# Optimization experiments

Hardware: AMD Instinct MI355X
Metric: run time of the kernel (lower is better)

The kernel has to match this reference:

```python
import jax, jax.numpy as jnp
import numpy as np

H = 128          # hidden_size == in_channels == graph_hidden_size
P = 16           # pair_neurons
B = 4096         # number of graph pairs
T = 262144       # total nodes per side
V_D, V_P, V_A = 10000, 4000, 4000          # leaf vocab sizes
NG_D, NG_P, NG_A = 13000, 5200, 5200       # DAG graph node counts
L_D, L_P, L_A = 4, 4, 5                    # ancestor levels
TOTAL_V = V_D + V_P + V_A                  # 18000 rows in all_embedding


def setup_inputs() -> dict:
    key = jax.random.key(0)
    ks = jax.random.split(key, 40)
    n = lambda i, shape, s: jax.random.normal(ks[i], shape, jnp.float32) * s
    ri = lambda i, shape, hi: jax.random.randint(ks[i], shape, 0, hi, dtype=jnp.int64)
    inp = {}
    # forward args
    inp["left_x"] = ri(0, (T, 1), TOTAL_V)
    inp["left_graph_index"] = ri(1, (B,), B)
    inp["right_x"] = ri(2, (T, 1), TOTAL_V)
    inp["right_graph_index"] = ri(3, (B,), B)
    inp["left_x_batch"] = jnp.sort(ri(4, (T,), B))
    inp["right_x_batch"] = jnp.sort(ri(5, (T,), B))
    inp["left_diag_cnt"] = ri(6, (B,), 64)
    inp["right_diag_cnt"] = ri(7, (B,), 64)
    # DAG structure buffers (built by build_ancestors in the original)
    inp["anc_d"] = ri(8, (V_D, L_D), NG_D)
    inp["leaf_d"] = ri(9, (V_D, L_D), NG_D)
    inp["anc_p"] = ri(10, (V_P, L_P), NG_P)
    inp["leaf_p"] = ri(11, (V_P, L_P), NG_P)
    inp["anc_a"] = ri(12, (V_A, L_A), NG_A)
    inp["leaf_a"] = ri(13, (V_A, L_A), NG_A)
    # learned parameters
    inp["emb_d"] = n(14, (NG_D, H), 0.1)
    inp["emb_p"] = n(15, (NG_P, H), 0.1)
    inp["emb_a"] = n(16, (NG_A, H), 0.1)
    inp["Wl_d"] = n(17, (H, 2 * H), 0.05); inp["bl_d"] = n(18, (H,), 0.05); inp["ap_d"] = n(19, (H, 1), 0.05)
    inp["Wl_p"] = n(20, (H, 2 * H), 0.05); inp["bl_p"] = n(21, (H,), 0.05); inp["ap_p"] = n(22, (H, 1), 0.05)
    inp["Wl_a"] = n(23, (H, 2 * H), 0.05); inp["bl_a"] = n(24, (H,), 0.05); inp["ap_a"] = n(25, (H, 1), 0.05)
    inp["W_ntn"] = n(26, (H, H, P), 0.02)
    inp["V_ntn"] = n(27, (P, 2 * H), 0.02)
    inp["b_ntn"] = n(28, (P,), 0.02)
    inp["w_fc"] = n(29, (1, P), 0.1)
    inp["b_fc"] = n(30, (1,), 0.1)
    return inp


def _dag_embedding(emb, anc, leaf, Wl, bl, ap):
    # emb: [Ng,H]; anc/leaf: [V,L] int
    anc_e = emb[anc]    # [V,L,H]
    leaf_e = emb[leaf]  # [V,L,H]
    h = jnp.tanh(jnp.concatenate([anc_e, leaf_e], axis=-1) @ Wl.T + bl)  # [V,L,H]
    aw = (h @ ap)[..., 0]                     # [V,L]
    s = jax.nn.softmax(aw, axis=-1)           # [V,L]
    # torch.matmul((V,L),(V,L,C)).sum(dim=1) == einsum('l,vlc->vc', s.sum(0), anc_e)
    return jnp.einsum('l,vlc->vc', s.sum(axis=0), anc_e)  # [V,H]


def reference(left_x, left_graph_index, right_x, right_graph_index,
              left_x_batch, right_x_batch, left_diag_cnt, right_diag_cnt,
              anc_d, leaf_d, anc_p, leaf_p, anc_a, leaf_a,
              emb_d, emb_p, emb_a,
              Wl_d, bl_d, ap_d, Wl_p, bl_p, ap_p, Wl_a, bl_a, ap_a,
              W_ntn, V_ntn, b_ntn, w_fc, b_fc):
    all_emb = jnp.concatenate([
        _dag_embedding(emb_d, anc_d, leaf_d, Wl_d, bl_d, ap_d),
        _dag_embedding(emb_p, anc_p, leaf_p, Wl_p, bl_p, ap_p),
        _dag_embedding(emb_a, anc_a, leaf_a, Wl_a, bl_a, ap_a),
    ], axis=0)                                  # [TOTAL_V, H]
    left_onto = all_emb[left_x[:, 0]]           # [T,H]
    right_onto = all_emb[right_x[:, 0]]         # [T,H]
    le = jax.ops.segment_sum(left_onto, left_x_batch, num_segments=B)    # [B,H]
    re = jax.ops.segment_sum(right_onto, right_x_batch, num_segments=B)  # [B,H]
    # Neural tensor similarity: tanh(e1^T W_k e2 + V [e1;e2] + b)
    bilinear = jnp.einsum('bi,ijp,bj->bp', le, W_ntn, re)                # [B,P]
    block = jnp.concatenate([le, re], axis=-1) @ V_ntn.T                 # [B,P]
    pair_sim = jnp.tanh(bilinear + block + b_ntn)                        # [B,P]
    out = jax.nn.sigmoid(pair_sim @ w_fc.T + b_fc)[:, 0]                 # [B]
    return out
```

## Files before the change

kernel.cpp:

```cpp
#include <hip/hip_runtime.h>
#include <hip/hip_bf16.h>

typedef __hip_bfloat16 bf16;
typedef __attribute__((ext_vector_type(8))) short bf16x8;
typedef __attribute__((ext_vector_type(4))) float f32x4;

#define HID 128
#define PD  16
#define BB  4096
#define TT  262144
#define VD  10000
#define VP  4000
#define VA  4000
#define NGD 13000
#define NGP 5200
#define NGA 5200

#define NB_D ((NGD + 31) / 32)
#define NB_P ((NGP + 31) / 32)
#define NB_A ((NGA + 31) / 32)

__device__ __forceinline__ float2 bf2x(unsigned int u) {
    float lo = __uint_as_float(u << 16);
    float hi = __uint_as_float(u & 0xffff0000u);
    return make_float2(lo, hi);
}

union Pack2 { bf16 h[2]; unsigned int u; };
__device__ __forceinline__ unsigned int pk2(float a, float b) {
    Pack2 p; p.h[0] = __float2bfloat16(a); p.h[1] = __float2bfloat16(b); return p.u;
}
__device__ __forceinline__ short bfs(float x) {
    bf16 h = __float2bfloat16(x);
    return *reinterpret_cast<short*>(&h);
}
union FragU { short s[8]; bf16x8 v; uint4 u; };

__global__ __launch_bounds__(256) void prologue(
    const float* __restrict__ Wl_d, const float* __restrict__ Wl_p, const float* __restrict__ Wl_a,
    bf16* __restrict__ B3_d, bf16* __restrict__ B3_p, bf16* __restrict__ B3_a,
    const int* __restrict__ lb, const int* __restrict__ rb,
    int* __restrict__ segL, int* __restrict__ segR, float* __restrict__ s_sum,
    const float* __restrict__ W2,
    bf16* __restrict__ W3h, bf16* __restrict__ W3m, bf16* __restrict__ W3l)
{
    __shared__ float LW[128][17];
    const int bx = blockIdx.x;
    const int tid = threadIdx.x;
    if (bx < 48) {
        const int sec = bx >> 4, jt = bx & 15;
        const float* Wl = (sec == 0) ? Wl_d : (sec == 1) ? Wl_p : Wl_a;
        bf16* B3 = (sec == 0) ? B3_d : (sec == 1) ? B3_p : B3_a;
        const int q = tid >> 6, lane = tid & 63;
        const int quad = lane >> 4, m = lane & 15;
        const int col = jt * 16 + m;
        const float* src = (col < 128) ? (Wl + col * 256) : (Wl + (col - 128) * 256 + 128);
        unsigned int pk[4];
#pragma unroll
        for (int jp = 0; jp < 4; ++jp) {
            int k0 = q * 32 + quad * 8 + 2 * jp;
            pk[jp] = pk2(src[k0], src[k0 + 1]);
        }
        uint4 val = make_uint4(pk[0], pk[1], pk[2], pk[3]);
        *reinterpret_cast<uint4*>(B3 + ((size_t)(jt * 4 + q) * 64 + lane) * 8) = val;
    } else if (bx < 81) {
        int gid = (bx - 48) * 256 + tid;
        if (gid >= 2 * BB + 8 && gid < 2 * BB + 24) s_sum[gid - (2 * BB + 8)] = 0.f;
        const int* batch;
        int* segp;
        int b;
        if (gid <= BB) { batch = lb; segp = segL; b = gid; }
        else if (gid <= 2 * BB + 1) { batch = rb; segp = segR; b = gid - BB - 1; }
        else return;
        int l = 0, r = TT;
        while (l < r) { int m2 = (l + r) >> 1; if (batch[m2] < b) l = m2 + 1; else r = m2; }
        segp[b] = l;
    } else {
        const int t = bx - 81;
        for (int idx = tid; idx < 2048; idx += 256) {
            int k = idx >> 4, m = idx & 15;
            LW[k][m] = W2[(size_t)k * 2048 + 16 * t + m];
        }
        __syncthreads();
        const int q = tid >> 6, lane = tid & 63;
        const int m = lane & 15, quad = lane >> 4;
        FragU fh, fm, fl;
#pragma unroll
        for (int j = 0; j < 8; ++j) {
            float x = LW[32 * q + quad * 8 + j][m];
            bf16 h = __float2bfloat16(x);
            float r = x - __bfloat162float(h);
            bf16 md = __float2bfloat16(r);
            float r2 = r - __bfloat162float(md);
            fh.s[j] = *reinterpret_cast<short*>(&h);
            fm.s[j] = *reinterpret_cast<short*>(&md);
            fl.s[j] = bfs(r2);
        }
        size_t off = ((size_t)(t * 4 + q) * 64 + lane) * 8;
        *reinterpret_cast<uint4*>(W3h + off) = fh.u;
        *reinterpret_cast<uint4*>(W3m + off) = fm.u;
        *reinterpret_cast<uint4*>(W3l + off) = fl.u;
    }
}

__device__ __forceinline__ void stage1_body(
    unsigned short (*Abf)[136],
    const float* __restrict__ emb, const bf16* __restrict__ B3,
    bf16* __restrict__ U, int NG, int blk)
{
    const int tid  = threadIdx.x;
    const int row0 = blk * 32;
    {
        const int r = tid >> 3, seg = tid & 7;
        const int g = row0 + r;
        float v[16];
        if (g < NG) {
            const float4* src = reinterpret_cast<const float4*>(emb + (size_t)g * HID + seg * 16);
#pragma unroll
            for (int i = 0; i < 4; ++i) {
                float4 f = src[i];
                v[4 * i] = f.x; v[4 * i + 1] = f.y; v[4 * i + 2] = f.z; v[4 * i + 3] = f.w;
            }
        } else {
#pragma unroll
            for (int i = 0; i < 16; ++i) v[i] = 0.f;
        }
        unsigned int pk[8];
#pragma unroll
        for (int i = 0; i < 8; ++i) pk[i] = pk2(v[2 * i], v[2 * i + 1]);
        uint4* dst = reinterpret_cast<uint4*>(&Abf[r][seg * 16]);
        dst[0] = make_uint4(pk[0], pk[1], pk[2], pk[3]);
        dst[1] = make_uint4(pk[4], pk[5], pk[6], pk[7]);
    }
    __syncthreads();

    const int lane   = tid & 63;
    const int w      = tid >> 6;
    const int gtile  = w & 1;
    const int jstrip = w >> 1;
    const int lrow   = gtile * 16 + (lane & 15);
    const int koff   = (lane >> 4) * 8;
    const bf16x8* B3f = reinterpret_cast<const bf16x8*>(B3);

    f32x4 acc[8];
#pragma unroll
    for (int t = 0; t < 8; ++t) acc[t] = (f32x4){0.f, 0.f, 0.f, 0.f};

#pragma unroll
    for (int q = 0; q < 4; ++q) {
        bf16x8 ef = *reinterpret_cast<const bf16x8*>(&Abf[lrow][q * 32 + koff]);
#pragma unroll
        for (int t = 0; t < 8; ++t) {
            int jt = jstrip * 8 + t;
            bf16x8 wf = B3f[(jt * 4 + q) * 64 + lane];
            acc[t] = __builtin_amdgcn_mfma_f32_16x16x32_bf16(wf, ef, acc[t], 0, 0, 0);
        }
    }

    const int g = row0 + gtile * 16 + (lane & 15);
    if (g < NG) {
        const int quad = lane >> 4;
        bf16* Ur = U + (size_t)g * 256;
#pragma unroll
        for (int t = 0; t < 8; ++t) {
            int j0 = (jstrip * 8 + t) * 16 + quad * 4;
            uint2 st = make_uint2(pk2(acc[t].x, acc[t].y), pk2(acc[t].z, acc[t].w));
            *reinterpret_cast<uint2*>(Ur + j0) = st;
        }
    }
}

__global__ __launch_bounds__(256) void stage1_mfma(
    const float* __restrict__ emb_d, const bf16* __restrict__ B3_d, bf16* __restrict__ U_d,
    const float* __restrict__ emb_p, const bf16* __restrict__ B3_p, bf16* __restrict__ U_p,
    const float* __restrict__ emb_a, const bf16* __restrict__ B3_a, bf16* __restrict__ U_a)
{
    __shared__ unsigned short Abf[32][136];
    int bx = blockIdx.x;
    if (bx < NB_D)             stage1_body(Abf, emb_d, B3_d, U_d, NGD, bx);
    else if (bx < NB_D + NB_P) stage1_body(Abf, emb_p, B3_p, U_p, NGP, bx - NB_D);
    else                       stage1_body(Abf, emb_a, B3_a, U_a, NGA, bx - NB_D - NB_P);
}

template <int L>
__device__ __forceinline__ void aw_body(
    float* sacc,
    const bf16* __restrict__ U, const int* __restrict__ anc, const int* __restrict__ leaf,
    const float* __restrict__ bl, const float* __restrict__ ap,
    float* __restrict__ s_out, int V, int blk, int nblk)
{
    const int tid  = threadIdx.x;
    const int lane = tid & 63;
    const int wid  = blk * 4 + (tid >> 6);
    const int nw   = nblk * 4;
    const float2 blv = *reinterpret_cast<const float2*>(bl + 2 * lane);
    const float2 apv = *reinterpret_cast<const float2*>(ap + 2 * lane);
    const unsigned int* Uw = reinterpret_cast<const unsigned int*>(U);
    float wacc[L];
#pragma unroll
    for (int l = 0; l < L; ++l) wacc[l] = 0.f;

    for (int vp = wid; vp < V / 2; vp += nw) {
        const int v0 = 2 * vp;
        int a0[L], f0[L], a1[L], f1[L];
        if (L == 4) {
            int4 ia = *reinterpret_cast<const int4*>(anc  + (size_t)v0 * 4);
            int4 ib = *reinterpret_cast<const int4*>(anc  + (size_t)v0 * 4 + 4);
            int4 fa = *reinterpret_cast<const int4*>(leaf + (size_t)v0 * 4);
            int4 fb = *reinterpret_cast<const int4*>(leaf + (size_t)v0 * 4 + 4);
            a0[0] = ia.x; a0[1] = ia.y; a0[2] = ia.z; a0[3] = ia.w;
            a1[0] = ib.x; a1[1] = ib.y; a1[2] = ib.z; a1[3] = ib.w;
            f0[0] = fa.x; f0[1] = fa.y; f0[2] = fa.z; f0[3] = fa.w;
            f1[0] = fb.x; f1[1] = fb.y; f1[2] = fb.z; f1[3] = fb.w;
        } else {
#pragma unroll
            for (int l = 0; l < L; ++l) {
                a0[l] = anc[(size_t)v0 * L + l];
                a1[l] = anc[(size_t)(v0 + 1) * L + l];
                f0[l] = leaf[(size_t)v0 * L + l];
                f1[l] = leaf[(size_t)(v0 + 1) * L + l];
            }
        }
        unsigned int ua0[L], ul0[L], ua1[L], ul1[L];
#pragma unroll
        for (int l = 0; l < L; ++l) {
            ua0[l] = Uw[(size_t)a0[l] * 128 + lane];
            ul0[l] = Uw[(size_t)f0[l] * 128 + 64 + lane];
            ua1[l] = Uw[(size_t)a1[l] * 128 + lane];
            ul1[l] = Uw[(size_t)f1[l] * 128 + 64 + lane];
        }
        float aw0[L], aw1[L];
#pragma unroll
        for (int l = 0; l < L; ++l) {
            float2 x0 = bf2x(ua0[l]), y0 = bf2x(ul0[l]);
            float2 x1 = bf2x(ua1[l]), y1 = bf2x(ul1[l]);
            float p0 = tanhf(x0.x + y0.x + blv.x) * apv.x + tanhf(x0.y + y0.y + blv.y) * apv.y;
            float p1 = tanhf(x1.x + y1.x + blv.x) * apv.x + tanhf(x1.y + y1.y + blv.y) * apv.y;
#pragma unroll
            for (int off = 32; off; off >>= 1) {
                p0 += __shfl_xor(p0, off, 64);
                p1 += __shfl_xor(p1, off, 64);
            }
            aw0[l] = p0; aw1[l] = p1;
        }
        float m0 = aw0[0], m1 = aw1[0];
#pragma unroll
        for (int l = 1; l < L; ++l) { m0 = fmaxf(m0, aw0[l]); m1 = fmaxf(m1, aw1[l]); }
        float d0 = 0.f, d1 = 0.f, e0[L], e1[L];
#pragma unroll
        for (int l = 0; l < L; ++l) {
            e0[l] = __expf(aw0[l] - m0); d0 += e0[l];
            e1[l] = __expf(aw1[l] - m1); d1 += e1[l];
        }
        float i0 = 1.f / d0, i1 = 1.f / d1;
#pragma unroll
        for (int l = 0; l < L; ++l) wacc[l] += e0[l] * i0 + e1[l] * i1;
    }
    if (lane == 0) {
#pragma unroll
        for (int l = 0; l < L; ++l) atomicAdd(&sacc[l], wacc[l]);
    }
    __syncthreads();
    if (tid < L) atomicAdd(&s_out[tid], sacc[tid]);
}

__global__ __launch_bounds__(256) void aw_all(
    const bf16* __restrict__ U_d, const int* __restrict__ anc_d, const int* __restrict__ leaf_d,
    const float* __restrict__ bl_d, const float* __restrict__ ap_d,
    const bf16* __restrict__ U_p, const int* __restrict__ anc_p, const int* __restrict__ leaf_p,
    const float* __restrict__ bl_p, const float* __restrict__ ap_p,
    const bf16* __restrict__ U_a, const int* __restrict__ anc_a, const int* __restrict__ leaf_a,
    const float* __restrict__ bl_a, const float* __restrict__ ap_a,
    float* __restrict__ s_sum)
{
    __shared__ float sacc[5];
    const int tid = threadIdx.x;
    if (tid < 5) sacc[tid] = 0.f;
    __syncthreads();
    int bx = blockIdx.x;
    if (bx < 512)      aw_body<4>(sacc, U_d, anc_d, leaf_d, bl_d, ap_d, s_sum + 0, VD, bx, 512);
    else if (bx < 768) aw_body<4>(sacc, U_p, anc_p, leaf_p, bl_p, ap_p, s_sum + 4, VP, bx - 512, 256);
    else               aw_body<5>(sacc, U_a, anc_a, leaf_a, bl_a, ap_a, s_sum + 8, VA, bx - 768, 256);
}

template <int L>
__device__ __forceinline__ void allemb_body(
    const float* __restrict__ emb, const int* __restrict__ anc,
    const float* __restrict__ s, float* __restrict__ out, int V, int blk, int nblk)
{
    const int tid   = threadIdx.x;
    const int lane4 = tid & 31;
    const int vslot = tid >> 5;
    const float4* emb4 = reinterpret_cast<const float4*>(emb);
    float4* out4 = reinterpret_cast<float4*>(out);
    float sv[L];
#pragma unroll
    for (int l = 0; l < L; ++l) sv[l] = s[l];
    for (int vp = blk * 8 + vslot; vp < V / 2; vp += nblk * 8) {
        const int v0 = 2 * vp;
        int a0[L], a1[L];
        if (L == 4) {
            int4 ia = *reinterpret_cast<const int4*>(anc + (size_t)v0 * 4);
            int4 ib = *reinterpret_cast<const int4*>(anc + (size_t)v0 * 4 + 4);
            a0[0] = ia.x; a0[1] = ia.y; a0[2] = ia.z; a0[3] = ia.w;
            a1[0] = ib.x; a1[1] = ib.y; a1[2] = ib.z; a1[3] = ib.w;
        } else {
#pragma unroll
            for (int l = 0; l < L; ++l) {
                a0[l] = anc[(size_t)v0 * L + l];
                a1[l] = anc[(size_t)(v0 + 1) * L + l];
            }
        }
        float4 e0[L], e1[L];
#pragma unroll
        for (int l = 0; l < L; ++l) {
            e0[l] = emb4[(size_t)a0[l] * 32 + lane4];
            e1[l] = emb4[(size_t)a1[l] * 32 + lane4];
        }
        float4 r0 = make_float4(0.f, 0.f, 0.f, 0.f);
        float4 r1 = make_float4(0.f, 0.f, 0.f, 0.f);
#pragma unroll
        for (int l = 0; l < L; ++l) {
            r0.x += sv[l] * e0[l].x; r0.y += sv[l] * e0[l].y;
            r0.z += sv[l] * e0[l].z; r0.w += sv[l] * e0[l].w;
            r1.x += sv[l] * e1[l].x; r1.y += sv[l] * e1[l].y;
            r1.z += sv[l] * e1[l].z; r1.w += sv[l] * e1[l].w;
        }
        out4[(size_t)v0 * 32 + lane4]       = r0;
        out4[(size_t)(v0 + 1) * 32 + lane4] = r1;
    }
}

__global__ __launch_bounds__(256) void allemb_all(
    const float* __restrict__ emb_d, const int* __restrict__ anc_d,
    const float* __restrict__ emb_p, const int* __restrict__ anc_p,
    const float* __restrict__ emb_a, const int* __restrict__ anc_a,
    const float* __restrict__ s_sum, float* __restrict__ all_emb)
{
    int bx = blockIdx.x;
    if (bx < 512)
        allemb_body<4>(emb_d, anc_d, s_sum + 0, all_emb, VD, bx, 512);
    else if (bx < 768)
        allemb_body<4>(emb_p, anc_p, s_sum + 4, all_emb + (size_t)VD * HID, VP, bx - 512, 256);
    else
        allemb_body<5>(emb_a, anc_a, s_sum + 8, all_emb + (size_t)(VD + VP) * HID, VA, bx - 768, 256);
}

__global__ __launch_bounds__(256) void segsum_mlp(
    const float* __restrict__ all_emb,
    const int* __restrict__ lx, const int* __restrict__ segL, float* __restrict__ le,
    const int* __restrict__ rx, const int* __restrict__ segR, float* __restrict__ re)
{
    __shared__ float4 red[4][32];
    const int tid  = threadIdx.x;
    const int b    = blockIdx.x & (BB - 1);
    const int lane = tid & 63;
    const int w    = tid >> 6;
    const int* x;
    const int* seg;
    float* out;
    if (blockIdx.x < BB) { x = lx; seg = segL; out = le; }
    else                 { x = rx; seg = segR; out = re; }
    const int lo = seg[b], hi = seg[b + 1];
    const int half  = lane >> 5;
    const int lane4 = lane & 31;
    const float4* AE4 = reinterpret_cast<const float4*>(all_emb);
    float4 acc = make_float4(0.f, 0.f, 0.f, 0.f);

    for (int tb = lo + 16 * w; tb < hi; tb += 64) {
        int idxv = x[min(tb + (lane & 15), hi - 1)];
        float4 v[8];
        int val[8];
#pragma unroll
        for (int u = 0; u < 8; ++u) {
            int src = 2 * u + half;
            int ridx = __shfl(idxv, src, 64);
            val[u] = (tb + src) < hi;
            v[u] = AE4[(size_t)ridx * 32 + lane4];
        }
#pragma unroll
        for (int u = 0; u < 8; ++u) {
            if (val[u]) {
                acc.x += v[u].x; acc.y += v[u].y;
                acc.z += v[u].z; acc.w += v[u].w;
            }
        }
    }
    acc.x += __shfl_xor(acc.x, 32, 64);
    acc.y += __shfl_xor(acc.y, 32, 64);
    acc.z += __shfl_xor(acc.z, 32, 64);
    acc.w += __shfl_xor(acc.w, 32, 64);
    if (lane < 32) red[w][lane4] = acc;
    __syncthreads();
    if (tid < 32) {
        float4 r0 = red[0][tid], r1 = red[1][tid], r2 = red[2][tid], r3 = red[3][tid];
        float4 s;
        s.x = r0.x + r1.x + r2.x + r3.x;
        s.y = r0.y + r1.y + r2.y + r3.y;
        s.z = r0.z + r1.z + r2.z + r3.z;
        s.w = r0.w + r1.w + r2.w + r3.w;
        reinterpret_cast<float4*>(out)[(size_t)b * 32 + tid] = s;
    }
}

__global__ __launch_bounds__(256) void ntn_mfma(
    const float* __restrict__ le, const float* __restrict__ re,
    const bf16* __restrict__ W3h, const bf16* __restrict__ W3m, const bf16* __restrict__ W3l,
    float* __restrict__ part)
{
    __shared__ float Rlds[64][17];
    const int tid  = threadIdx.x;
    const int bg   = blockIdx.x;
    const int ch   = blockIdx.y;
    const int w    = tid >> 6;
    const int lane = tid & 63;
    const int m    = lane & 15;
    const int quad = lane >> 4;
    const int rb   = bg * 64 + w * 16 + m;

    for (int idx = tid; idx < 1024; idx += 256) {
        int row = idx >> 4, jl = idx & 15;
        Rlds[row][jl] = re[(size_t)(bg * 64 + row) * HID + ch * 16 + jl];
    }

    bf16x8 lh[4], lm[4], ll[4];
    {
        const float* lp = le + (size_t)rb * HID + quad * 8;
#pragma unroll
        for (int q = 0; q < 4; ++q) {
            float4 f0 = *reinterpret_cast<const float4*>(lp + 32 * q);
            float4 f1 = *reinterpret_cast<const float4*>(lp + 32 * q + 4);
            float x[8] = {f0.x, f0.y, f0.z, f0.w, f1.x, f1.y, f1.z, f1.w};
            FragU fh, fm, fl;
#pragma unroll
            for (int j = 0; j < 8; ++j) {
                bf16 h = __float2bfloat16(x[j]);
                float r = x[j] - __bfloat162float(h);
                bf16 md = __float2bfloat16(r);
                float r2 = r - __bfloat162float(md);
                fh.s[j] = *reinterpret_cast<short*>(&h);
                fm.s[j] = *reinterpret_cast<short*>(&md);
                fl.s[j] = bfs(r2);
            }
            lh[q] = fh.v; lm[q] = fm.v; ll[q] = fl.v;
        }
    }
    __syncthreads();

    const bf16x8* Whf = reinterpret_cast<const bf16x8*>(W3h);
    const bf16x8* Wmf = reinterpret_cast<const bf16x8*>(W3m);
    const bf16x8* Wlf = reinterpret_cast<const bf16x8*>(W3l);

    float blin[4] = {0.f, 0.f, 0.f, 0.f};
#pragma unroll 2
    for (int tl = 0; tl < 16; ++tl) {
        const int t = ch * 16 + tl;
        f32x4 acc = (f32x4){0.f, 0.f, 0.f, 0.f};
#pragma unroll
        for (int q = 0; q < 4; ++q) {
            const int fi = (t * 4 + q) * 64 + lane;
            bf16x8 wh = Whf[fi], wm = Wmf[fi], wl = Wlf[fi];
            acc = __builtin_amdgcn_mfma_f32_16x16x32_bf16(wh, lh[q], acc, 0, 0, 0);
            acc = __builtin_amdgcn_mfma_f32_16x16x32_bf16(wh, lm[q], acc, 0, 0, 0);
            acc = __builtin_amdgcn_mfma_f32_16x16x32_bf16(wm, lh[q], acc, 0, 0, 0);
            acc = __builtin_amdgcn_mfma_f32_16x16x32_bf16(wh, ll[q], acc, 0, 0, 0);
            acc = __builtin_amdgcn_mfma_f32_16x16x32_bf16(wl, lh[q], acc, 0, 0, 0);
            acc = __builtin_amdgcn_mfma_f32_16x16x32_bf16(wm, lm[q], acc, 0, 0, 0);
        }
        float rt = Rlds[w * 16 + m][tl];
        blin[0] += acc.x * rt;
        blin[1] += acc.y * rt;
        blin[2] += acc.z * rt;
        blin[3] += acc.w * rt;
    }

    size_t base = ((size_t)ch * BB + rb) * PD + quad * 4;
    *reinterpret_cast<float4*>(&part[base]) = make_float4(blin[0], blin[1], blin[2], blin[3]);
}

__global__ __launch_bounds__(256) void ntn_epi(
    const float* __restrict__ part, const float* __restrict__ le, const float* __restrict__ re,
    const float* __restrict__ Vntn, const float* __restrict__ bntn,
    const float* __restrict__ wfc, const float* __restrict__ bfc,
    float* __restrict__ out)
{
    __shared__ float Vlds[16 * 257];
    __shared__ float LE[16 * 128];
    __shared__ float RE[16 * 128];
    const int tid = threadIdx.x;
    const int b0  = blockIdx.x * 16;
    for (int i = tid; i < 4096; i += 256) Vlds[(i >> 8) * 257 + (i & 255)] = Vntn[i];
    for (int i = tid; i < 2048; i += 256) {
        LE[i] = le[(size_t)b0 * HID + i];
        RE[i] = re[(size_t)b0 * HID + i];
    }
    __syncthreads();
    const int bl = tid >> 4, p = tid & 15;
    const int b  = b0 + bl;
    float bil = 0.f;
#pragma unroll
    for (int by = 0; by < 8; ++by) bil += part[((size_t)by * BB + b) * PD + p];
    float s = bil + bntn[p];
    const float* Vp   = &Vlds[p * 257];
    const float* lrow = &LE[bl * 128];
    const float* rrow = &RE[bl * 128];
#pragma unroll 8
    for (int c = 0; c < 128; ++c) s += lrow[c] * Vp[c] + rrow[c] * Vp[128 + c];
    float x = tanhf(s) * wfc[p];
    x += __shfl_xor(x, 1, 64);
    x += __shfl_xor(x, 2, 64);
    x += __shfl_xor(x, 4, 64);
    x += __shfl_xor(x, 8, 64);
    if (p == 0) out[b] = 1.f / (1.f + __expf(-(x + bfc[0])));
}

extern "C" void kernel_launch(void* const* d_in, const int* in_sizes, int n_in,
                              void* d_out, int out_size, void* d_ws, size_t ws_size,
                              hipStream_t stream)
{
    const int* left_x      = (const int*)d_in[0];
    const int* right_x     = (const int*)d_in[2];
    const int* left_batch  = (const int*)d_in[4];
    const int* right_batch = (const int*)d_in[5];
    const int* anc_d  = (const int*)d_in[8];
    const int* leaf_d = (const int*)d_in[9];
    const int* anc_p  = (const int*)d_in[10];
    const int* leaf_p = (const int*)d_in[11];
    const int* anc_a  = (const int*)d_in[12];
    const int* leaf_a = (const int*)d_in[13];
    const float* emb_d = (const float*)d_in[14];
    const float* emb_p = (const float*)d_in[15];
    const float* emb_a = (const float*)d_in[16];
    const float* Wl_d = (const float*)d_in[17];
    const float* bl_d = (const float*)d_in[18];
    const float* ap_d = (const float*)d_in[19];
    const float* Wl_p = (const float*)d_in[20];
    const float* bl_p = (const float*)d_in[21];
    const float* ap_p = (const float*)d_in[22];
    const float* Wl_a = (const float*)d_in[23];
    const float* bl_a = (const float*)d_in[24];
    const float* ap_a = (const float*)d_in[25];
    const float* W_ntn = (const float*)d_in[26];
    const float* V_ntn = (const float*)d_in[27];
    const float* b_ntn = (const float*)d_in[28];
    const float* w_fc  = (const float*)d_in[29];
    const float* b_fc  = (const float*)d_in[30];
    float* out = (float*)d_out;

    float* ws = (float*)d_ws;
    float* s_sum   = ws;
    float* le      = ws + 64;
    float* re      = le + (size_t)BB * HID;
    float* all_emb = re + (size_t)BB * HID;
    float* part    = all_emb + (size_t)(VD + VP + VA) * HID;
    int*   segL    = (int*)(part + (size_t)8 * BB * PD);
    int*   segR    = segL + 4100;
    bf16*  U       = (bf16*)(segR + 4100);
    bf16*  U_d = U;
    bf16*  U_p = U_d + (size_t)NGD * 256;
    bf16*  U_a = U_p + (size_t)NGP * 256;
    bf16*  B3_d = U_a + (size_t)NGA * 256;
    bf16*  B3_p = B3_d + 32768;
    bf16*  B3_a = B3_p + 32768;
    bf16*  W3h  = B3_a + 32768;
    bf16*  W3m  = W3h + 262144;
    bf16*  W3l  = W3m + 262144;

    prologue<<<209, 256, 0, stream>>>(
        Wl_d, Wl_p, Wl_a, B3_d, B3_p, B3_a,
        left_batch, right_batch, segL, segR, s_sum,
        W_ntn, W3h, W3m, W3l);

    stage1_mfma<<<NB_D + NB_P + NB_A, 256, 0, stream>>>(
        emb_d, B3_d, U_d, emb_p, B3_p, U_p, emb_a, B3_a, U_a);

    aw_all<<<1024, 256, 0, stream>>>(
        U_d, anc_d, leaf_d, bl_d, ap_d,
        U_p, anc_p, leaf_p, bl_p, ap_p,
        U_a, anc_a, leaf_a, bl_a, ap_a, s_sum);

    allemb_all<<<1024, 256, 0, stream>>>(
        emb_d, anc_d, emb_p, anc_p, emb_a, anc_a, s_sum, all_emb);

    segsum_mlp<<<2 * BB, 256, 0, stream>>>(
        all_emb, left_x, segL, le, right_x, segR, re);

    ntn_mfma<<<dim3(64, 8), 256, 0, stream>>>(le, re, W3h, W3m, W3l, part);

    ntn_epi<<<BB / 16, 256, 0, stream>>>(part, le, re, V_ntn, b_ntn, w_fc, b_fc, out);
}
```

Measured before the change: 223.5 us.

## Partition segment-sum gathers by vocab slice per XCD with atomic accumulation

Replaces the per-segment gather-sum kernel with one that launches 8 blocks per graph. Each block handles only the node indices that fall into one eighth of the embedding table, so consecutive blocks land on different XCDs and each XCD's L2 holds only its own slice of all_emb. Partial sums are combined with float atomics into le/re, which the prologue now zeroes with extra blocks. The cost is that every block re-reads all node indices, branches more, and issues atomics, and the float summation order is no longer deterministic.

```diff
diff --git a/kernel.cpp b/kernel.cpp
--- a/kernel.cpp
+++ b/kernel.cpp
@@ -15,6 +15,8 @@
 #define NGD 13000
 #define NGP 5200
 #define NGA 5200
+#define VTOT (VD + VP + VA)
+#define SLICE_ROWS (VTOT / 8)
 
 #define NB_D ((NGD + 31) / 32)
 #define NB_P ((NGP + 31) / 32)
@@ -42,7 +44,8 @@
     const int* __restrict__ lb, const int* __restrict__ rb,
     int* __restrict__ segL, int* __restrict__ segR, float* __restrict__ s_sum,
     const float* __restrict__ W2,
-    bf16* __restrict__ W3h, bf16* __restrict__ W3m, bf16* __restrict__ W3l)
+    bf16* __restrict__ W3h, bf16* __restrict__ W3m, bf16* __restrict__ W3l,
+    float* __restrict__ lere)
 {
     __shared__ float LW[128][17];
     const int bx = blockIdx.x;
@@ -75,7 +78,7 @@
         int l = 0, r = TT;
         while (l < r) { int m2 = (l + r) >> 1; if (batch[m2] < b) l = m2 + 1; else r = m2; }
         segp[b] = l;
-    } else {
+    } else if (bx < 209) {
         const int t = bx - 81;
         for (int idx = tid; idx < 2048; idx += 256) {
             int k = idx >> 4, m = idx & 15;
@@ -100,6 +103,12 @@
         *reinterpret_cast<uint4*>(W3h + off) = fh.u;
         *reinterpret_cast<uint4*>(W3m + off) = fm.u;
         *reinterpret_cast<uint4*>(W3l + off) = fl.u;
+    } else {
+        float4* p = reinterpret_cast<float4*>(lere);
+        int base = (bx - 209) * 256 + tid;
+        float4 z = make_float4(0.f, 0.f, 0.f, 0.f);
+#pragma unroll
+        for (int i = 0; i < 16; ++i) p[base + i * 16384] = z;
     }
 }
 
@@ -346,60 +355,50 @@
         allemb_body<5>(emb_a, anc_a, s_sum + 8, all_emb + (size_t)(VD + VP) * HID, VA, bx - 768, 256);
 }
 
-__global__ __launch_bounds__(256) void segsum_mlp(
+__global__ __launch_bounds__(128) void segsum_xcd(
     const float* __restrict__ all_emb,
     const int* __restrict__ lx, const int* __restrict__ segL, float* __restrict__ le,
     const int* __restrict__ rx, const int* __restrict__ segR, float* __restrict__ re)
 {
     __shared__ float4 red[4][32];
-    const int tid  = threadIdx.x;
-    const int b    = blockIdx.x & (BB - 1);
-    const int lane = tid & 63;
-    const int w    = tid >> 6;
-    const int* x;
-    const int* seg;
-    float* out;
-    if (blockIdx.x < BB) { x = lx; seg = segL; out = le; }
-    else                 { x = rx; seg = segR; out = re; }
-    const int lo = seg[b], hi = seg[b + 1];
-    const int half  = lane >> 5;
-    const int lane4 = lane & 31;
+    const int tid   = threadIdx.x;
+    const int b     = blockIdx.x >> 3;
+    const int s     = blockIdx.x & 7;
+    const int v0    = s * SLICE_ROWS;
+    const int v1    = v0 + SLICE_ROWS;
+    const int lane4 = tid & 31;
+    const int slot  = tid >> 5;
     const float4* AE4 = reinterpret_cast<const float4*>(all_emb);
-    float4 acc = make_float4(0.f, 0.f, 0.f, 0.f);
-
-    for (int tb = lo + 16 * w; tb < hi; tb += 64) {
-        int idxv = x[min(tb + (lane & 15), hi - 1)];
-        float4 v[8];
-        int val[8];
-#pragma unroll
-        for (int u = 0; u < 8; ++u) {
-            int src = 2 * u + half;
-            int ridx = __shfl(idxv, src, 64);
-            val[u] = (tb + src) < hi;
-            v[u] = AE4[(size_t)ridx * 32 + lane4];
-        }
-#pragma unroll
-        for (int u = 0; u < 8; ++u) {
-            if (val[u]) {
-                acc.x += v[u].x; acc.y += v[u].y;
-                acc.z += v[u].z; acc.w += v[u].w;
+
+#pragma unroll
+    for (int side = 0; side < 2; ++side) {
+        const int* x   = side ? rx : lx;
+        const int* seg = side ? segR : segL;
+        float* out     = side ? re : le;
+        const int lo = seg[b], hi = seg[b + 1];
+        float4 acc = make_float4(0.f, 0.f, 0.f, 0.f);
+        for (int t = lo + slot; t < hi; t += 4) {
+            int idx = x[t];
+            if (idx >= v0 && idx < v1) {
+                float4 v = AE4[(size_t)idx * 32 + lane4];
+                acc.x += v.x; acc.y += v.y; acc.z += v.z; acc.w += v.w;
             }
         }
-    }
-    acc.x += __shfl_xor(acc.x, 32, 64);
-    acc.y += __shfl_xor(acc.y, 32, 64);
-    acc.z += __shfl_xor(acc.z, 32, 64);
-    acc.w += __shfl_xor(acc.w, 32, 64);
-    if (lane < 32) red[w][lane4] = acc;
-    __syncthreads();
-    if (tid < 32) {
-        float4 r0 = red[0][tid], r1 = red[1][tid], r2 = red[2][tid], r3 = red[3][tid];
-        float4 s;
-        s.x = r0.x + r1.x + r2.x + r3.x;
-        s.y = r0.y + r1.y + r2.y + r3.y;
-        s.z = r0.z + r1.z + r2.z + r3.z;
-        s.w = r0.w + r1.w + r2.w + r3.w;
-        reinterpret_cast<float4*>(out)[(size_t)b * 32 + tid] = s;
+        red[slot][lane4] = acc;
+        __syncthreads();
+        if (slot == 0) {
+            float4 r1 = red[1][lane4], r2 = red[2][lane4], r3 = red[3][lane4];
+            acc.x += r1.x + r2.x + r3.x;
+            acc.y += r1.y + r2.y + r3.y;
+            acc.z += r1.z + r2.z + r3.z;
+            acc.w += r1.w + r2.w + r3.w;
+            float* dst = out + (size_t)b * HID + lane4 * 4;
+            atomicAdd(dst + 0, acc.x);
+            atomicAdd(dst + 1, acc.y);
+            atomicAdd(dst + 2, acc.z);
+            atomicAdd(dst + 3, acc.w);
+        }
+        __syncthreads();
     }
 }
 
@@ -552,7 +551,7 @@
     float* le      = ws + 64;
     float* re      = le + (size_t)BB * HID;
     float* all_emb = re + (size_t)BB * HID;
-    float* part    = all_emb + (size_t)(VD + VP + VA) * HID;
+    float* part    = all_emb + (size_t)VTOT * HID;
     int*   segL    = (int*)(part + (size_t)8 * BB * PD);
     int*   segR    = segL + 4100;
     bf16*  U       = (bf16*)(segR + 4100);
@@ -566,10 +565,10 @@
     bf16*  W3m  = W3h + 262144;
     bf16*  W3l  = W3m + 262144;
 
-    prologue<<<209, 256, 0, stream>>>(
+    prologue<<<273, 256, 0, stream>>>(
         Wl_d, Wl_p, Wl_a, B3_d, B3_p, B3_a,
         left_batch, right_batch, segL, segR, s_sum,
-        W_ntn, W3h, W3m, W3l);
+        W_ntn, W3h, W3m, W3l, le);
 
     stage1_mfma<<<NB_D + NB_P + NB_A, 256, 0, stream>>>(
         emb_d, B3_d, U_d, emb_p, B3_p, U_p, emb_a, B3_a, U_a);
@@ -582,7 +581,7 @@
     allemb_all<<<1024, 256, 0, stream>>>(
         emb_d, anc_d, emb_p, anc_p, emb_a, anc_a, s_sum, all_emb);
 
-    segsum_mlp<<<2 * BB, 256, 0, stream>>>(
+    segsum_xcd<<<BB * 8, 128, 0, stream>>>(
         all_emb, left_x, segL, le, right_x, segR, re);
 
     ntn_mfma<<<dim3(64, 8), 256, 0, stream>>>(le, re, W3h, W3m, W3l, part);
```

After: 338.3 us. 1.51x slower.
